# Performance work log

Hardware: AMD Instinct MI355X
Metric: run time of the kernel (lower is better)

Reference implementation:

```python
import jax, jax.numpy as jnp
import numpy as np

BS1, BS2, NUM_EC = 32, 128, 64
CONV_DIM, MEM_DIM, MLP_DIM = 64, 256, 256
Q_DIM = 4 * CONV_DIM  # query_dim of criteria


def setup_inputs() -> dict:
    key = jax.random.key(0)
    k = jax.random.split(key, 6)
    in_dim = Q_DIM + MEM_DIM
    s_a = 1.0 / np.sqrt(in_dim)
    return {
        "ehr_vector": jax.random.normal(k[0], (BS2, MEM_DIM), dtype=jnp.float32),
        "criteria": jax.random.normal(k[1], (BS1, NUM_EC, Q_DIM), dtype=jnp.float32),
        "ec_mask": jnp.ones((BS1, NUM_EC), dtype=jnp.float32),
        # alignment: Linear(mem_dim + 4*conv_dim, 1) -> store as [in_dim] vector + scalar bias
        "W_align": jax.random.normal(k[2], (in_dim,), dtype=jnp.float32) * s_a,
        "b_align": jax.random.normal(k[3], (1,), dtype=jnp.float32) * s_a,
        # mlp: Linear(mem_dim + 4*conv_dim, mlp_dim) -> store as [in_dim, mlp_dim]
        "W_mlp": jax.random.normal(k[4], (in_dim, MLP_DIM), dtype=jnp.float32) * s_a,
        "b_mlp": jax.random.normal(k[5], (MLP_DIM,), dtype=jnp.float32) * s_a,
    }


def reference(ehr_vector, criteria, ec_mask, W_align, b_align, W_mlp, b_mlp):
    # Math identical to: att = softmax(Linear(cat[criteria, ehr]), dim=ec);
    # h = Linear_mlp(cat[criteria, ehr] * att). Concat is never materialized:
    # split both linear weights along the input dim instead.
    q = criteria.shape[-1]
    Wa_c, Wa_e = W_align[:q], W_align[q:]
    # additive attention logits: [bs1, bs2, num_ec]
    logit_c = jnp.einsum("beq,q->be", criteria, Wa_c)      # [bs1, num_ec]
    logit_e = jnp.einsum("pm,m->p", ehr_vector, Wa_e)      # [bs2]
    logits = logit_c[:, None, :] + logit_e[None, :, None] + b_align[0]
    att = jax.nn.softmax(logits, axis=2)                   # softmax over num_ec

    Wm_c, Wm_e = W_mlp[:q], W_mlp[q:]
    proj_c = jnp.einsum("beq,qd->bed", criteria, Wm_c)     # [bs1, num_ec, mlp]
    proj_e = jnp.einsum("pm,md->pd", ehr_vector, Wm_e)     # [bs2, mlp]
    # mlp((cat * att)) = att * (cat @ W_mlp) + b_mlp  (att is scalar per (b,p,e))
    h = att[..., None] * (proj_c[:, None, :, :] + proj_e[None, :, None, :]) + b_mlp
    return h  # [bs1, bs2, num_ec, mlp_dim]
```

## Files before the change

### kernel.cpp

```cpp
#include <hip/hip_runtime.h>

#define BS1 32
#define BS2 128
#define NEC 64
#define QD  256
#define MD  256

__global__ __launch_bounds__(64)
void att_kernel(const float* __restrict__ crit,
                const float* __restrict__ w_align,
                float* __restrict__ att) {
    __shared__ float wa[QD];
    int b = blockIdx.x, e = threadIdx.x;
    for (int i = e; i < QD; i += 64) wa[i] = w_align[i];
    __syncthreads();
    const float* row = crit + (b * NEC + e) * QD;
    float acc = 0.f;
    for (int k = 0; k < QD; k += 4) {
        float4 u = *(const float4*)(row + k);
        acc = fmaf(u.x, wa[k + 0], acc);
        acc = fmaf(u.y, wa[k + 1], acc);
        acc = fmaf(u.z, wa[k + 2], acc);
        acc = fmaf(u.w, wa[k + 3], acc);
    }
    float m = acc;
    #pragma unroll
    for (int off = 32; off; off >>= 1) m = fmaxf(m, __shfl_xor(m, off));
    float ex = __expf(acc - m);
    float s = ex;
    #pragma unroll
    for (int off = 32; off; off >>= 1) s += __shfl_xor(s, off);
    att[b * NEC + e] = ex / s;
}

__global__ __launch_bounds__(256)
void gemm_rows8(const float* __restrict__ A,
                const float* __restrict__ B,
                float* __restrict__ out) {
    __shared__ float As[8 * QD];
    int tid = threadIdx.x;
    int m0 = blockIdx.x * 8;
    {
        const float* src = A + m0 * QD + tid * 8;
        float4 a0 = *(const float4*)src;
        float4 a1 = *(const float4*)(src + 4);
        *(float4*)&As[tid * 8]     = a0;
        *(float4*)&As[tid * 8 + 4] = a1;
    }
    __syncthreads();
    int r = tid >> 5;
    int c = (tid & 31) * 8;
    float acc[8] = {0.f,0.f,0.f,0.f,0.f,0.f,0.f,0.f};
    #pragma unroll 4
    for (int k = 0; k < QD; ++k) {
        float a = As[r * QD + k];
        const float* bp = B + k * MD + c;
        float4 b0 = *(const float4*)bp;
        float4 b1 = *(const float4*)(bp + 4);
        acc[0] = fmaf(a, b0.x, acc[0]);
        acc[1] = fmaf(a, b0.y, acc[1]);
        acc[2] = fmaf(a, b0.z, acc[2]);
        acc[3] = fmaf(a, b0.w, acc[3]);
        acc[4] = fmaf(a, b1.x, acc[4]);
        acc[5] = fmaf(a, b1.y, acc[5]);
        acc[6] = fmaf(a, b1.z, acc[6]);
        acc[7] = fmaf(a, b1.w, acc[7]);
    }
    float* o = out + (m0 + r) * MD + c;
    *(float4*)o       = make_float4(acc[0], acc[1], acc[2], acc[3]);
    *(float4*)(o + 4) = make_float4(acc[4], acc[5], acc[6], acc[7]);
}

__global__ __launch_bounds__(256)
void final_kernel(const float* __restrict__ att,
                  const float* __restrict__ proj_c,
                  const float* __restrict__ proj_e,
                  const float* __restrict__ b_mlp,
                  float*       __restrict__ out) {
    __shared__ float pe[MD], bm[MD], attb[NEC];
    int tid = threadIdx.x;
    int bp  = blockIdx.x;
    int b = bp >> 7, p = bp & 127;
    pe[tid] = proj_e[p * MD + tid];
    bm[tid] = b_mlp[tid];
    if (tid < NEC) attb[tid] = att[b * NEC + tid];
    __syncthreads();
    const float* pc_base = proj_c + b * NEC * MD;
    float* out_base = out + (size_t)bp * (NEC * MD);
    #pragma unroll
    for (int pass = 0; pass < 8; ++pass) {
        int idx = pass * 256 + tid;
        int e = idx >> 5;
        int d = (idx & 31) * 8;
        float a = attb[e];
        const float* pc = pc_base + e * MD + d;
        float4 c0 = *(const float4*)pc;
        float4 c1 = *(const float4*)(pc + 4);
        float4 e0 = *(const float4*)&pe[d];
        float4 e1 = *(const float4*)&pe[d + 4];
        float4 m0 = *(const float4*)&bm[d];
        float4 m1 = *(const float4*)&bm[d + 4];
        float4 r0, r1;
        r0.x = fmaf(a, c0.x + e0.x, m0.x);
        r0.y = fmaf(a, c0.y + e0.y, m0.y);
        r0.z = fmaf(a, c0.z + e0.z, m0.z);
        r0.w = fmaf(a, c0.w + e0.w, m0.w);
        r1.x = fmaf(a, c1.x + e1.x, m1.x);
        r1.y = fmaf(a, c1.y + e1.y, m1.y);
        r1.z = fmaf(a, c1.z + e1.z, m1.z);
        r1.w = fmaf(a, c1.w + e1.w, m1.w);
        float* o = out_base + (size_t)idx * 8;
        *(float4*)o       = r0;
        *(float4*)(o + 4) = r1;
    }
}

extern "C" void kernel_launch(void* const* d_in, const int* in_sizes, int n_in,
                              void* d_out, int out_size, void* d_ws, size_t ws_size,
                              hipStream_t stream) {
    const float* ehr     = (const float*)d_in[0];
    const float* crit    = (const float*)d_in[1];
    const float* w_align = (const float*)d_in[3];
    const float* w_mlp   = (const float*)d_in[5];
    const float* b_mlp   = (const float*)d_in[6];
    float* out = (float*)d_out;

    float* att    = (float*)d_ws;
    float* proj_c = att + BS1 * NEC;
    float* proj_e = proj_c + BS1 * NEC * MD;

    att_kernel<<<BS1, 64, 0, stream>>>(crit, w_align, att);
    gemm_rows8<<<(BS1 * NEC) / 8, 256, 0, stream>>>(crit, w_mlp, proj_c);
    gemm_rows8<<<BS2 / 8, 256, 0, stream>>>(ehr, w_mlp + QD * MD, proj_e);
    final_kernel<<<BS1 * BS2, 256, 0, stream>>>(att, proj_c, proj_e, b_mlp, out);
}
```

Measured before the change: 352.0 us.

## Merge attention and projection GEMMs into one launch; nontemporal output stores

Combines the attention-softmax kernel and both projection GEMMs into a single prework kernel that selects its role by block index, cutting launches from four to two. In the final kernel, proj_e and b_mlp are now read straight into registers instead of staged in shared memory, since each thread uses one fixed column slice. The 64 MB output is written with nontemporal stores to keep it from polluting the cache. The output write dominates, so most of the expected benefit comes from the stores and fewer launches, and the gain may be modest.

```diff
diff --git a/kernel.cpp b/kernel.cpp
--- a/kernel.cpp
+++ b/kernel.cpp
@@ -6,69 +6,78 @@
 #define QD  256
 #define MD  256
 
-__global__ __launch_bounds__(64)
-void att_kernel(const float* __restrict__ crit,
-                const float* __restrict__ w_align,
-                float* __restrict__ att) {
-    __shared__ float wa[QD];
-    int b = blockIdx.x, e = threadIdx.x;
-    for (int i = e; i < QD; i += 64) wa[i] = w_align[i];
-    __syncthreads();
-    const float* row = crit + (b * NEC + e) * QD;
-    float acc = 0.f;
-    for (int k = 0; k < QD; k += 4) {
-        float4 u = *(const float4*)(row + k);
-        acc = fmaf(u.x, wa[k + 0], acc);
-        acc = fmaf(u.y, wa[k + 1], acc);
-        acc = fmaf(u.z, wa[k + 2], acc);
-        acc = fmaf(u.w, wa[k + 3], acc);
-    }
-    float m = acc;
-    #pragma unroll
-    for (int off = 32; off; off >>= 1) m = fmaxf(m, __shfl_xor(m, off));
-    float ex = __expf(acc - m);
-    float s = ex;
-    #pragma unroll
-    for (int off = 32; off; off >>= 1) s += __shfl_xor(s, off);
-    att[b * NEC + e] = ex / s;
-}
+typedef float nf4 __attribute__((ext_vector_type(4)));
 
 __global__ __launch_bounds__(256)
-void gemm_rows8(const float* __restrict__ A,
-                const float* __restrict__ B,
-                float* __restrict__ out) {
+void prework_kernel(const float* __restrict__ crit,
+                    const float* __restrict__ ehr,
+                    const float* __restrict__ w_align,
+                    const float* __restrict__ w_mlp,
+                    float* __restrict__ proj_c,
+                    float* __restrict__ proj_e,
+                    float* __restrict__ att) {
     __shared__ float As[8 * QD];
+    int blk = blockIdx.x;
     int tid = threadIdx.x;
-    int m0 = blockIdx.x * 8;
-    {
-        const float* src = A + m0 * QD + tid * 8;
-        float4 a0 = *(const float4*)src;
-        float4 a1 = *(const float4*)(src + 4);
-        *(float4*)&As[tid * 8]     = a0;
-        *(float4*)&As[tid * 8 + 4] = a1;
+
+    if (blk < 272) {
+        const float* A;
+        const float* B;
+        float*       O;
+        int m0;
+        if (blk < 256) { A = crit; B = w_mlp;           O = proj_c; m0 = blk * 8; }
+        else           { A = ehr;  B = w_mlp + QD * MD; O = proj_e; m0 = (blk - 256) * 8; }
+        {
+            const float* src = A + m0 * QD + tid * 8;
+            float4 a0 = *(const float4*)src;
+            float4 a1 = *(const float4*)(src + 4);
+            *(float4*)&As[tid * 8]     = a0;
+            *(float4*)&As[tid * 8 + 4] = a1;
+        }
+        __syncthreads();
+        int r = tid >> 5;
+        int c = (tid & 31) * 8;
+        float acc[8] = {0.f,0.f,0.f,0.f,0.f,0.f,0.f,0.f};
+        #pragma unroll 4
+        for (int k = 0; k < QD; ++k) {
+            float a = As[r * QD + k];
+            const float* bp = B + k * MD + c;
+            float4 b0 = *(const float4*)bp;
+            float4 b1 = *(const float4*)(bp + 4);
+            acc[0] = fmaf(a, b0.x, acc[0]);
+            acc[1] = fmaf(a, b0.y, acc[1]);
+            acc[2] = fmaf(a, b0.z, acc[2]);
+            acc[3] = fmaf(a, b0.w, acc[3]);
+            acc[4] = fmaf(a, b1.x, acc[4]);
+            acc[5] = fmaf(a, b1.y, acc[5]);
+            acc[6] = fmaf(a, b1.z, acc[6]);
+            acc[7] = fmaf(a, b1.w, acc[7]);
+        }
+        float* o = O + (m0 + r) * MD + c;
+        *(float4*)o       = make_float4(acc[0], acc[1], acc[2], acc[3]);
+        *(float4*)(o + 4) = make_float4(acc[4], acc[5], acc[6], acc[7]);
+    } else {
+        if (tid >= 64) return;
+        int b = blk - 272;
+        int e = tid;
+        const float* row = crit + (b * NEC + e) * QD;
+        float acc = 0.f;
+        for (int k = 0; k < QD; k += 4) {
+            float4 u = *(const float4*)(row + k);
+            acc = fmaf(u.x, w_align[k + 0], acc);
+            acc = fmaf(u.y, w_align[k + 1], acc);
+            acc = fmaf(u.z, w_align[k + 2], acc);
+            acc = fmaf(u.w, w_align[k + 3], acc);
+        }
+        float m = acc;
+        #pragma unroll
+        for (int off = 32; off; off >>= 1) m = fmaxf(m, __shfl_xor(m, off));
+        float ex = __expf(acc - m);
+        float s = ex;
+        #pragma unroll
+        for (int off = 32; off; off >>= 1) s += __shfl_xor(s, off);
+        att[b * NEC + e] = ex / s;
     }
-    __syncthreads();
-    int r = tid >> 5;
-    int c = (tid & 31) * 8;
-    float acc[8] = {0.f,0.f,0.f,0.f,0.f,0.f,0.f,0.f};
-    #pragma unroll 4
-    for (int k = 0; k < QD; ++k) {
-        float a = As[r * QD + k];
-        const float* bp = B + k * MD + c;
-        float4 b0 = *(const float4*)bp;
-        float4 b1 = *(const float4*)(bp + 4);
-        acc[0] = fmaf(a, b0.x, acc[0]);
-        acc[1] = fmaf(a, b0.y, acc[1]);
-        acc[2] = fmaf(a, b0.z, acc[2]);
-        acc[3] = fmaf(a, b0.w, acc[3]);
-        acc[4] = fmaf(a, b1.x, acc[4]);
-        acc[5] = fmaf(a, b1.y, acc[5]);
-        acc[6] = fmaf(a, b1.z, acc[6]);
-        acc[7] = fmaf(a, b1.w, acc[7]);
-    }
-    float* o = out + (m0 + r) * MD + c;
-    *(float4*)o       = make_float4(acc[0], acc[1], acc[2], acc[3]);
-    *(float4*)(o + 4) = make_float4(acc[4], acc[5], acc[6], acc[7]);
 }
 
 __global__ __launch_bounds__(256)
@@ -77,30 +86,31 @@
                   const float* __restrict__ proj_e,
                   const float* __restrict__ b_mlp,
                   float*       __restrict__ out) {
-    __shared__ float pe[MD], bm[MD], attb[NEC];
+    __shared__ float attb[NEC];
     int tid = threadIdx.x;
     int bp  = blockIdx.x;
     int b = bp >> 7, p = bp & 127;
-    pe[tid] = proj_e[p * MD + tid];
-    bm[tid] = b_mlp[tid];
+    int d = (tid & 31) * 8;
+
     if (tid < NEC) attb[tid] = att[b * NEC + tid];
+
+    float4 e0 = *(const float4*)(proj_e + p * MD + d);
+    float4 e1 = *(const float4*)(proj_e + p * MD + d + 4);
+    float4 m0 = *(const float4*)(b_mlp + d);
+    float4 m1 = *(const float4*)(b_mlp + d + 4);
     __syncthreads();
+
     const float* pc_base = proj_c + b * NEC * MD;
     float* out_base = out + (size_t)bp * (NEC * MD);
     #pragma unroll
     for (int pass = 0; pass < 8; ++pass) {
         int idx = pass * 256 + tid;
-        int e = idx >> 5;
-        int d = (idx & 31) * 8;
+        int e = pass * 8 + (tid >> 5);
         float a = attb[e];
         const float* pc = pc_base + e * MD + d;
         float4 c0 = *(const float4*)pc;
         float4 c1 = *(const float4*)(pc + 4);
-        float4 e0 = *(const float4*)&pe[d];
-        float4 e1 = *(const float4*)&pe[d + 4];
-        float4 m0 = *(const float4*)&bm[d];
-        float4 m1 = *(const float4*)&bm[d + 4];
-        float4 r0, r1;
+        nf4 r0, r1;
         r0.x = fmaf(a, c0.x + e0.x, m0.x);
         r0.y = fmaf(a, c0.y + e0.y, m0.y);
         r0.z = fmaf(a, c0.z + e0.z, m0.z);
@@ -109,9 +119,9 @@
         r1.y = fmaf(a, c1.y + e1.y, m1.y);
         r1.z = fmaf(a, c1.z + e1.z, m1.z);
         r1.w = fmaf(a, c1.w + e1.w, m1.w);
-        float* o = out_base + (size_t)idx * 8;
-        *(float4*)o       = r0;
-        *(float4*)(o + 4) = r1;
+        nf4* o = (nf4*)(out_base + (size_t)idx * 8);
+        __builtin_nontemporal_store(r0, o);
+        __builtin_nontemporal_store(r1, o + 1);
     }
 }
 
@@ -129,8 +139,7 @@
     float* proj_c = att + BS1 * NEC;
     float* proj_e = proj_c + BS1 * NEC * MD;
 
-    att_kernel<<<BS1, 64, 0, stream>>>(crit, w_align, att);
-    gemm_rows8<<<(BS1 * NEC) / 8, 256, 0, stream>>>(crit, w_mlp, proj_c);
-    gemm_rows8<<<BS2 / 8, 256, 0, stream>>>(ehr, w_mlp + QD * MD, proj_e);
+    prework_kernel<<<272 + BS1, 256, 0, stream>>>(crit, ehr, w_align, w_mlp,
+                                                  proj_c, proj_e, att);
     final_kernel<<<BS1 * BS2, 256, 0, stream>>>(att, proj_c, proj_e, b_mlp, out);
 }
```

After: 378.1 us. 1.07x slower.
